# Kernel tuning notes

Hardware: AMD Instinct MI355X
Metric: run time of the kernel (lower is better)

The kernel has to match this reference:

```python
import jax, jax.numpy as jnp
import numpy as np

NUM_GRAPHS = 512  # number of segments (graphs) in the batch
NEG_SLOPE = 0.01  # nn.LeakyReLU default


def setup_inputs() -> dict:
    key = jax.random.key(0)
    k1, k2, k3, k4, k5 = jax.random.split(key, 5)
    N, D = 200000, 128
    h_topo = jax.random.normal(k1, (N, D), dtype=jnp.float32)
    h_geom = jax.random.normal(k2, (N, D), dtype=jnp.float32)
    batch = jnp.sort(jax.random.randint(k3, (N,), 0, NUM_GRAPHS, dtype=jnp.int64))
    concat_dim, hidden, out_dim = 6 * D, 2 * D, 128
    W1 = jax.random.normal(k4, (concat_dim, hidden), dtype=jnp.float32) * 0.02
    b1 = jnp.zeros((hidden,), dtype=jnp.float32)
    W2 = jax.random.normal(k5, (hidden, out_dim), dtype=jnp.float32) * 0.02
    b2 = jnp.zeros((out_dim,), dtype=jnp.float32)
    return {"h_topo": h_topo, "h_geom": h_geom, "batch": batch,
            "W1": W1, "b1": b1, "W2": W2, "b2": b2}


def _pool_feats(h, batch):
    # global_max_pool / global_mean_pool keyed by graph id, gathered back per node
    gmax = jax.ops.segment_max(h, batch, num_segments=NUM_GRAPHS)
    gsum = jax.ops.segment_sum(h, batch, num_segments=NUM_GRAPHS)
    cnt = jax.ops.segment_sum(jnp.ones((h.shape[0],), h.dtype), batch,
                              num_segments=NUM_GRAPHS)
    gmean = gsum / jnp.maximum(cnt, 1.0)[:, None]
    return gmax[batch], gmean[batch]  # [N, D] each


def reference(h_topo, h_geom, batch, W1, b1, W2, b2):
    t_max, t_mean = _pool_feats(h_topo, batch)
    g_max, g_mean = _pool_feats(h_geom, batch)
    # [Topo, Geom, TopoMax, TopoMean, GeomMax, GeomMean]
    combined = jnp.concatenate(
        [h_topo, t_max, t_mean, h_geom, g_max, g_mean], axis=-1)  # [N, 6D]
    h = combined @ W1 + b1
    h = jnp.where(h >= 0, h, NEG_SLOPE * h)  # LeakyReLU
    return h @ W2 + b2
```

## Files before the change

### kernel.cpp

```cpp
#include <hip/hip_runtime.h>
#include <math.h>

#define NUM_GRAPHS 512
#define D 128
#define NEG 0.01f
#define BN 128
#define NS 4

typedef __attribute__((ext_vector_type(8))) short  bf16x8;
typedef __attribute__((ext_vector_type(4))) float  f32x4;

__device__ __forceinline__ unsigned short f2bf(float f) {
    unsigned u = __float_as_uint(f);
    u += 0x7fffu + ((u >> 16) & 1u);
    return (unsigned short)(u >> 16);
}

__device__ __forceinline__ uint2 pack4(float4 v) {
    uint2 pk;
    pk.x = (unsigned)f2bf(v.x) | ((unsigned)f2bf(v.y) << 16);
    pk.y = (unsigned)f2bf(v.z) | ((unsigned)f2bf(v.w) << 16);
    return pk;
}

__device__ __forceinline__ int swz(int row, int k) {
    return row * 256 + (k ^ ((row & 7) << 3));
}
__device__ __forceinline__ int swz128(int row, int k) {
    return (row >> 6) * 16384 + (row & 63) * 256 + (k ^ ((row & 7) << 3));
}

#define GLD16(gsrc, ldst)                                                    \
    __builtin_amdgcn_global_load_lds(                                        \
        (const __attribute__((address_space(1))) void*)(gsrc),               \
        (__attribute__((address_space(3))) void*)(ldst), 16, 0, 0)

#define LDS_BARRIER()                                                        \
    do {                                                                     \
        asm volatile("s_waitcnt lgkmcnt(0)" ::: "memory");                   \
        __builtin_amdgcn_s_barrier();                                        \
        asm volatile("" ::: "memory");                                       \
    } while (0)

#define FMAX4(a, b)                                                          \
    do {                                                                     \
        (a).x = fmaxf((a).x, (b).x); (a).y = fmaxf((a).y, (b).y);            \
        (a).z = fmaxf((a).z, (b).z); (a).w = fmaxf((a).w, (b).w);            \
    } while (0)
#define FADD4(a, b)                                                          \
    do {                                                                     \
        (a).x += (b).x; (a).y += (b).y; (a).z += (b).z; (a).w += (b).w;      \
    } while (0)

__global__ __launch_bounds__(256) void bounds_kernel(
    const int* __restrict__ batch, int N, int* __restrict__ seg)
{
    const int g = blockIdx.x * 256 + threadIdx.x;
    if (g <= NUM_GRAPHS) {
        int lo = 0, hi = N;
        while (lo < hi) { int m = (lo + hi) >> 1; if (batch[m] < g) lo = m + 1; else hi = m; }
        seg[g] = lo;
    }
}

__global__ __launch_bounds__(256) void pool_kernel(
    const float* __restrict__ h_topo, const float* __restrict__ h_geom,
    const int* __restrict__ seg, int N, float* __restrict__ pp,
    unsigned short* __restrict__ xt)
{
    const int g = blockIdx.x, t = blockIdx.y, s = blockIdx.z;
    const float* __restrict__ h = t ? h_geom : h_topo;
    const int koff = t ? 128 : 0;

    const int start = seg[g], end = seg[g + 1];
    const int len = end - start;
    const int r0  = start + (int)(((long long)len * s) / NS);
    const int r1  = start + (int)(((long long)len * (s + 1)) / NS);

    const int c = threadIdx.x & 31;
    const int r = threadIdx.x >> 5;
    const int kk = koff + c * 4;

    float4 mxA = make_float4(-INFINITY, -INFINITY, -INFINITY, -INFINITY);
    float4 mxB = mxA, mxC = mxA, mxD = mxA;
    float4 smA = make_float4(0.f, 0.f, 0.f, 0.f);
    float4 smB = smA, smC = smA, smD = smA;

    int row = r0 + r;
    for (; row + 24 < r1; row += 32) {
        float4 v0 = *(const float4*)(h + (size_t)row * D + c * 4);
        float4 v1 = *(const float4*)(h + (size_t)(row + 8)  * D + c * 4);
        float4 v2 = *(const float4*)(h + (size_t)(row + 16) * D + c * 4);
        float4 v3 = *(const float4*)(h + (size_t)(row + 24) * D + c * 4);
        FMAX4(mxA, v0); FADD4(smA, v0);
        FMAX4(mxB, v1); FADD4(smB, v1);
        FMAX4(mxC, v2); FADD4(smC, v2);
        FMAX4(mxD, v3); FADD4(smD, v3);
        *(uint2*)(xt + (size_t)(row >> 6) * 16384 + swz(row & 63, kk)) = pack4(v0);
        *(uint2*)(xt + (size_t)((row + 8)  >> 6) * 16384 + swz((row + 8)  & 63, kk)) = pack4(v1);
        *(uint2*)(xt + (size_t)((row + 16) >> 6) * 16384 + swz((row + 16) & 63, kk)) = pack4(v2);
        *(uint2*)(xt + (size_t)((row + 24) >> 6) * 16384 + swz((row + 24) & 63, kk)) = pack4(v3);
    }
    for (; row < r1; row += 8) {
        float4 v = *(const float4*)(h + (size_t)row * D + c * 4);
        FMAX4(mxA, v); FADD4(smA, v);
        *(uint2*)(xt + (size_t)(row >> 6) * 16384 + swz(row & 63, kk)) = pack4(v);
    }
    FMAX4(mxA, mxB); FMAX4(mxC, mxD); FMAX4(mxA, mxC);
    FADD4(smA, smB); FADD4(smC, smD); FADD4(smA, smC);

    __shared__ float4 smx[256], ssm[256];
    smx[threadIdx.x] = mxA; ssm[threadIdx.x] = smA;
    __syncthreads();
    #pragma unroll
    for (int st = 4; st > 0; st >>= 1) {
        if (r < st) {
            float4 a = smx[threadIdx.x + st * 32];
            float4 b = ssm[threadIdx.x + st * 32];
            float4 m0 = smx[threadIdx.x];
            float4 s0 = ssm[threadIdx.x];
            FMAX4(m0, a); FADD4(s0, b);
            smx[threadIdx.x] = m0; ssm[threadIdx.x] = s0;
        }
        __syncthreads();
    }
    if (r == 0) {
        float* dst = pp + ((size_t)(g * 2 + t) * NS + s) * 256;
        *(float4*)(dst + c * 4)       = smx[threadIdx.x];
        *(float4*)(dst + 128 + c * 4) = ssm[threadIdx.x];
    }
}

__global__ __launch_bounds__(256) void pmat_kernel(
    const float* __restrict__ pp, const int* __restrict__ seg,
    const float* __restrict__ W1, const float* __restrict__ b1,
    float* __restrict__ P)
{
    const int g = blockIdx.x;
    const int j = threadIdx.x;

    const int start = seg[g], end = seg[g + 1];
    const float inv   = 1.0f / fmaxf((float)(end - start), 1.0f);
    const bool  empty = (end <= start);

    __shared__ float pl[512];
    #pragma unroll
    for (int e0 = 0; e0 < 2; ++e0) {
        const int e = j + e0 * 256;
        const int t = e >> 8, i = e & 255;
        const float* q = pp + (size_t)(g * 2 + t) * NS * 256 + i;
        float v;
        if (i < 128)
            v = fmaxf(fmaxf(q[0], q[256]), fmaxf(q[512], q[768]));
        else
            v = (q[0] + q[256] + q[512] + q[768]) * inv;
        pl[e] = empty ? 0.f : v;
    }
    __syncthreads();

    float acc = b1[j];
    #pragma unroll 8
    for (int k = 0; k < 256; ++k)
        acc += pl[k] * W1[(size_t)(128 + k) * 256 + j];
    #pragma unroll 8
    for (int k = 0; k < 256; ++k)
        acc += pl[256 + k] * W1[(size_t)(512 + k) * 256 + j];

    P[(size_t)g * 256 + j] = acc;
}

__global__ __launch_bounds__(256) void wconv_kernel(
    const float* __restrict__ W1, const float* __restrict__ W2,
    unsigned short* __restrict__ W1bT, unsigned short* __restrict__ W2bT)
{
    const int idx = blockIdx.x * 256 + threadIdx.x;
    if (idx < 256 * 256) {
        const int n = idx >> 8, k = idx & 255;
        const int kk = (k < 128) ? k : (k + 256);
        W1bT[idx] = f2bf(W1[(size_t)kk * 256 + n]);
    } else {
        const int j = idx - 256 * 256;
        if (j < 128 * 256) {
            const int n = j >> 8, k = j & 255;
            W2bT[j] = f2bf(W2[(size_t)k * 128 + n]);
        }
    }
}

__global__ __launch_bounds__(512, 4) void mlp_mfma(
    const unsigned short* __restrict__ xt, const int* __restrict__ batch,
    const float* __restrict__ P,
    const unsigned short* __restrict__ W1bT, const unsigned short* __restrict__ W2bT,
    const float* __restrict__ b2, float* __restrict__ out, int N)
{
    __shared__ unsigned short xs[128 * 256];
    __shared__ int gid[128];

    const int tid  = threadIdx.x;
    const int wave = tid >> 6, lane = tid & 63;
    const int base = blockIdx.x * BN;
    const size_t tbase = (size_t)blockIdx.x * 32768;

    const int nchunk = (base + 64 < N) ? 8 : 4;
    for (int c = 0; c < nchunk; ++c) {
        const int off = (c * 512 + tid) * 8;
        GLD16(xt + tbase + off, xs + off);
    }
    if (tid < 128) gid[tid] = batch[min(base + tid, N - 1)];

    const int g0 = batch[base];
    const int g1 = batch[min(base + 127, N - 1)];
    const bool uni = (g0 == g1);

    const int lhi = lane >> 4;
    const int llo = lane & 15;

    const unsigned short* w1p = W1bT + (size_t)(wave * 32 + llo) * 256 + lhi * 8;
    const unsigned short* w2p = W2bT + (size_t)(wave * 16 + llo) * 256 + lhi * 8;

    float pf[2];
    if (uni) {
        #pragma unroll
        for (int ct = 0; ct < 2; ++ct)
            pf[ct] = P[(size_t)g0 * 256 + wave * 32 + ct * 16 + llo];
    }

    bf16x8 bfr[2][2];
    #pragma unroll
    for (int ct = 0; ct < 2; ++ct) {
        bfr[0][ct] = *(const bf16x8*)(w1p + (size_t)ct * 16 * 256);
        bfr[1][ct] = *(const bf16x8*)(w1p + (size_t)ct * 16 * 256 + 32);
    }

    asm volatile("s_waitcnt vmcnt(0)" ::: "memory");
    __syncthreads();

    f32x4 acc[8][2];
    #pragma unroll
    for (int rt = 0; rt < 8; ++rt)
        #pragma unroll
        for (int ct = 0; ct < 2; ++ct) {
            const float p = uni ? pf[ct] : 0.f;
            acc[rt][ct] = (f32x4){p, p, p, p};
        }

    #pragma unroll
    for (int ks = 0; ks < 8; ++ks) {
        const int kb = ks * 32 + lhi * 8;
        bf16x8 afr[8];
        #pragma unroll
        for (int rt = 0; rt < 8; ++rt)
            afr[rt] = *(const bf16x8*)&xs[swz128(rt * 16 + llo, kb)];
        __builtin_amdgcn_s_setprio(1);
        #pragma unroll
        for (int rt = 0; rt < 8; ++rt)
            #pragma unroll
            for (int ct = 0; ct < 2; ++ct)
                acc[rt][ct] = __builtin_amdgcn_mfma_f32_16x16x32_bf16(
                    afr[rt], bfr[ks & 1][ct], acc[rt][ct], 0, 0, 0);
        __builtin_amdgcn_s_setprio(0);
        if (ks < 6) {
            const int kbn = (ks + 2) * 32;
            #pragma unroll
            for (int ct = 0; ct < 2; ++ct)
                bfr[ks & 1][ct] = *(const bf16x8*)(w1p + (size_t)ct * 16 * 256 + kbn);
        }
    }

    bf16x8 bfr2[2];
    bfr2[0] = *(const bf16x8*)(w2p);
    bfr2[1] = *(const bf16x8*)(w2p + 32);

    LDS_BARRIER();

    #pragma unroll
    for (int rt = 0; rt < 8; ++rt) {
        #pragma unroll
        for (int ct = 0; ct < 2; ++ct) {
            const int col = wave * 32 + ct * 16 + llo;
            #pragma unroll
            for (int q = 0; q < 4; ++q) {
                const int row = rt * 16 + lhi * 4 + q;
                float v = acc[rt][ct][q];
                if (!uni) v += P[(size_t)gid[row] * 256 + col];
                v = fmaxf(v, NEG * v);
                xs[swz128(row, col)] = f2bf(v);
            }
        }
    }

    LDS_BARRIER();

    f32x4 acc2[8];
    {
        const float bv = b2[wave * 16 + llo];
        #pragma unroll
        for (int rt = 0; rt < 8; ++rt)
            acc2[rt] = (f32x4){bv, bv, bv, bv};
    }
    #pragma unroll
    for (int ks = 0; ks < 8; ++ks) {
        const int kb = ks * 32 + lhi * 8;
        bf16x8 afr[8];
        #pragma unroll
        for (int rt = 0; rt < 8; ++rt)
            afr[rt] = *(const bf16x8*)&xs[swz128(rt * 16 + llo, kb)];
        __builtin_amdgcn_s_setprio(1);
        #pragma unroll
        for (int rt = 0; rt < 8; ++rt)
            acc2[rt] = __builtin_amdgcn_mfma_f32_16x16x32_bf16(
                afr[rt], bfr2[ks & 1], acc2[rt], 0, 0, 0);
        __builtin_amdgcn_s_setprio(0);
        if (ks < 6)
            bfr2[ks & 1] = *(const bf16x8*)(w2p + (ks + 2) * 32);
    }

    #pragma unroll
    for (int rt = 0; rt < 8; ++rt)
        #pragma unroll
        for (int q = 0; q < 4; ++q) {
            const int row  = rt * 16 + lhi * 4 + q;
            const int node = base + row;
            if (node < N)
                out[(size_t)node * 128 + wave * 16 + llo] = acc2[rt][q];
        }
}

extern "C" void kernel_launch(void* const* d_in, const int* in_sizes, int n_in,
                              void* d_out, int out_size, void* d_ws, size_t ws_size,
                              hipStream_t stream)
{
    const float* h_topo = (const float*)d_in[0];
    const float* h_geom = (const float*)d_in[1];
    const int*   batch  = (const int*)  d_in[2];
    const float* W1     = (const float*)d_in[3];
    const float* b1     = (const float*)d_in[4];
    const float* W2     = (const float*)d_in[5];
    const float* b2     = (const float*)d_in[6];
    float* out = (float*)d_out;

    const int N = in_sizes[0] / D;

    float*          pp   = (float*)d_ws;
    float*          P    = pp + (size_t)NUM_GRAPHS * 2 * NS * 256;
    unsigned short* W1bT = (unsigned short*)(P + (size_t)NUM_GRAPHS * 256);
    unsigned short* W2bT = W1bT + 256 * 256;
    int*            seg  = (int*)(W2bT + 128 * 256);

    const size_t small_bytes = (size_t)NUM_GRAPHS * 2 * NS * 256 * 4
                             + (size_t)NUM_GRAPHS * 256 * 4
                             + (size_t)(256 * 256 + 128 * 256) * 2
                             + 1024 * 4;
    const size_t xt_bytes = (size_t)N * 256 * 2;

    unsigned short* xt;
    if (ws_size >= small_bytes + xt_bytes)
        xt = (unsigned short*)((char*)d_ws + small_bytes);
    else
        xt = (unsigned short*)d_out;

    bounds_kernel<<<3, 256, 0, stream>>>(batch, N, seg);
    wconv_kernel<<<(256 * 256 + 128 * 256) / 256, 256, 0, stream>>>(W1, W2, W1bT, W2bT);
    pool_kernel<<<dim3(NUM_GRAPHS, 2, NS), 256, 0, stream>>>(h_topo, h_geom, seg, N,
                                                             pp, xt);
    pmat_kernel<<<NUM_GRAPHS, 256, 0, stream>>>(pp, seg, W1, b1, P);

    const int nblocks = (N + BN - 1) / BN;
    mlp_mfma<<<nblocks, 512, 0, stream>>>(xt, batch, P, W1bT, W2bT, b2, out, N);
}
```

Before: 200.0 us.

## Fuse bf16 conversion into MLP kernel, drop intermediate bf16 activation buffer

The pooling kernel no longer writes a swizzled bf16 copy of the node features. The MLP kernel instead loads fp32 rows of h_topo and h_geom directly, converts them with packed bf16 conversion instructions, and stores them swizzled into LDS. This removes the intermediate buffer's write and re-read and the scattered 8-byte stores in the pool pass. In exchange the MLP kernel reads twice as many bytes per tile and loses the async global-to-LDS load path.

```diff
diff --git a/kernel.cpp b/kernel.cpp
--- a/kernel.cpp
+++ b/kernel.cpp
@@ -9,6 +9,7 @@
 
 typedef __attribute__((ext_vector_type(8))) short  bf16x8;
 typedef __attribute__((ext_vector_type(4))) float  f32x4;
+typedef __attribute__((ext_vector_type(4))) int    i32x4;
 
 __device__ __forceinline__ unsigned short f2bf(float f) {
     unsigned u = __float_as_uint(f);
@@ -16,24 +17,19 @@
     return (unsigned short)(u >> 16);
 }
 
-__device__ __forceinline__ uint2 pack4(float4 v) {
-    uint2 pk;
-    pk.x = (unsigned)f2bf(v.x) | ((unsigned)f2bf(v.y) << 16);
-    pk.y = (unsigned)f2bf(v.z) | ((unsigned)f2bf(v.w) << 16);
-    return pk;
-}
-
-__device__ __forceinline__ int swz(int row, int k) {
-    return row * 256 + (k ^ ((row & 7) << 3));
-}
+__device__ __forceinline__ bf16x8 cvt8(float4 a, float4 b) {
+    unsigned w0, w1, w2, w3;
+    asm("v_cvt_pk_bf16_f32 %0, %1, %2" : "=v"(w0) : "v"(a.x), "v"(a.y));
+    asm("v_cvt_pk_bf16_f32 %0, %1, %2" : "=v"(w1) : "v"(a.z), "v"(a.w));
+    asm("v_cvt_pk_bf16_f32 %0, %1, %2" : "=v"(w2) : "v"(b.x), "v"(b.y));
+    asm("v_cvt_pk_bf16_f32 %0, %1, %2" : "=v"(w3) : "v"(b.z), "v"(b.w));
+    i32x4 v; v[0] = (int)w0; v[1] = (int)w1; v[2] = (int)w2; v[3] = (int)w3;
+    return __builtin_bit_cast(bf16x8, v);
+}
+
 __device__ __forceinline__ int swz128(int row, int k) {
     return (row >> 6) * 16384 + (row & 63) * 256 + (k ^ ((row & 7) << 3));
 }
-
-#define GLD16(gsrc, ldst)                                                    \
-    __builtin_amdgcn_global_load_lds(                                        \
-        (const __attribute__((address_space(1))) void*)(gsrc),               \
-        (__attribute__((address_space(3))) void*)(ldst), 16, 0, 0)
 
 #define LDS_BARRIER()                                                        \
     do {                                                                     \
@@ -65,12 +61,10 @@
 
 __global__ __launch_bounds__(256) void pool_kernel(
     const float* __restrict__ h_topo, const float* __restrict__ h_geom,
-    const int* __restrict__ seg, int N, float* __restrict__ pp,
-    unsigned short* __restrict__ xt)
+    const int* __restrict__ seg, int N, float* __restrict__ pp)
 {
     const int g = blockIdx.x, t = blockIdx.y, s = blockIdx.z;
     const float* __restrict__ h = t ? h_geom : h_topo;
-    const int koff = t ? 128 : 0;
 
     const int start = seg[g], end = seg[g + 1];
     const int len = end - start;
@@ -79,7 +73,6 @@
 
     const int c = threadIdx.x & 31;
     const int r = threadIdx.x >> 5;
-    const int kk = koff + c * 4;
 
     float4 mxA = make_float4(-INFINITY, -INFINITY, -INFINITY, -INFINITY);
     float4 mxB = mxA, mxC = mxA, mxD = mxA;
@@ -96,15 +89,10 @@
         FMAX4(mxB, v1); FADD4(smB, v1);
         FMAX4(mxC, v2); FADD4(smC, v2);
         FMAX4(mxD, v3); FADD4(smD, v3);
-        *(uint2*)(xt + (size_t)(row >> 6) * 16384 + swz(row & 63, kk)) = pack4(v0);
-        *(uint2*)(xt + (size_t)((row + 8)  >> 6) * 16384 + swz((row + 8)  & 63, kk)) = pack4(v1);
-        *(uint2*)(xt + (size_t)((row + 16) >> 6) * 16384 + swz((row + 16) & 63, kk)) = pack4(v2);
-        *(uint2*)(xt + (size_t)((row + 24) >> 6) * 16384 + swz((row + 24) & 63, kk)) = pack4(v3);
     }
     for (; row < r1; row += 8) {
         float4 v = *(const float4*)(h + (size_t)row * D + c * 4);
         FMAX4(mxA, v); FADD4(smA, v);
-        *(uint2*)(xt + (size_t)(row >> 6) * 16384 + swz(row & 63, kk)) = pack4(v);
     }
     FMAX4(mxA, mxB); FMAX4(mxC, mxD); FMAX4(mxA, mxC);
     FADD4(smA, smB); FADD4(smC, smD); FADD4(smA, smC);
@@ -188,8 +176,8 @@
 }
 
 __global__ __launch_bounds__(512, 4) void mlp_mfma(
-    const unsigned short* __restrict__ xt, const int* __restrict__ batch,
-    const float* __restrict__ P,
+    const float* __restrict__ h_topo, const float* __restrict__ h_geom,
+    const int* __restrict__ batch, const float* __restrict__ P,
     const unsigned short* __restrict__ W1bT, const unsigned short* __restrict__ W2bT,
     const float* __restrict__ b2, float* __restrict__ out, int N)
 {
@@ -199,12 +187,18 @@
     const int tid  = threadIdx.x;
     const int wave = tid >> 6, lane = tid & 63;
     const int base = blockIdx.x * BN;
-    const size_t tbase = (size_t)blockIdx.x * 32768;
-
-    const int nchunk = (base + 64 < N) ? 8 : 4;
-    for (int c = 0; c < nchunk; ++c) {
-        const int off = (c * 512 + tid) * 8;
-        GLD16(xt + tbase + off, xs + off);
+
+    {
+        const int row  = tid >> 2, kq = tid & 3;
+        const int node = min(base + row, N - 1);
+        const float* src = (kq < 2) ? h_topo + (size_t)node * D + kq * 64
+                                    : h_geom + (size_t)node * D + (kq - 2) * 64;
+        #pragma unroll
+        for (int i = 0; i < 8; ++i) {
+            float4 a = ((const float4*)src)[2 * i];
+            float4 b = ((const float4*)src)[2 * i + 1];
+            *(bf16x8*)&xs[swz128(row, kq * 64 + i * 8)] = cvt8(a, b);
+        }
     }
     if (tid < 128) gid[tid] = batch[min(base + tid, N - 1)];
 
@@ -232,8 +226,7 @@
         bfr[1][ct] = *(const bf16x8*)(w1p + (size_t)ct * 16 * 256 + 32);
     }
 
-    asm volatile("s_waitcnt vmcnt(0)" ::: "memory");
-    __syncthreads();
+    LDS_BARRIER();
 
     f32x4 acc[8][2];
     #pragma unroll
@@ -347,24 +340,12 @@
     unsigned short* W2bT = W1bT + 256 * 256;
     int*            seg  = (int*)(W2bT + 128 * 256);
 
-    const size_t small_bytes = (size_t)NUM_GRAPHS * 2 * NS * 256 * 4
-                             + (size_t)NUM_GRAPHS * 256 * 4
-                             + (size_t)(256 * 256 + 128 * 256) * 2
-                             + 1024 * 4;
-    const size_t xt_bytes = (size_t)N * 256 * 2;
-
-    unsigned short* xt;
-    if (ws_size >= small_bytes + xt_bytes)
-        xt = (unsigned short*)((char*)d_ws + small_bytes);
-    else
-        xt = (unsigned short*)d_out;
-
     bounds_kernel<<<3, 256, 0, stream>>>(batch, N, seg);
     wconv_kernel<<<(256 * 256 + 128 * 256) / 256, 256, 0, stream>>>(W1, W2, W1bT, W2bT);
-    pool_kernel<<<dim3(NUM_GRAPHS, 2, NS), 256, 0, stream>>>(h_topo, h_geom, seg, N,
-                                                             pp, xt);
+    pool_kernel<<<dim3(NUM_GRAPHS, 2, NS), 256, 0, stream>>>(h_topo, h_geom, seg, N, pp);
     pmat_kernel<<<NUM_GRAPHS, 256, 0, stream>>>(pp, seg, W1, b1, P);
 
     const int nblocks = (N + BN - 1) / BN;
-    mlp_mfma<<<nblocks, 512, 0, stream>>>(xt, batch, P, W1bT, W2bT, b2, out, N);
-}
+    mlp_mfma<<<nblocks, 512, 0, stream>>>(h_topo, h_geom, batch, P,
+                                          W1bT, W2bT, b2, out, N);
+}
```

Measured after the change: 192.7 us. -3.7%, faster.
